# Kernel tuning notes

Hardware: AMD Instinct MI355X
Metric: run time of the kernel (lower is better)

## Reference

```python
import jax, jax.numpy as jnp
import numpy as np

# Module hyperparameters (init kwargs)
QUALITY_W = 1.0
UNCERT_W = 0.5
STEP_PEN = 0.1
EARLY_BONUS = 0.5
LATE_PEN = 0.3
ORTHO_W = 1.0

B = 8388608  # batch
MAX_STEPS = 20


def setup_inputs() -> dict:
    key = jax.random.key(0)
    ks = jax.random.split(key, 6)
    return {
        "current_quality": jax.random.uniform(ks[0], (B,), dtype=jnp.float32),
        "previous_quality": jax.random.uniform(ks[1], (B,), dtype=jnp.float32),
        "uncertainty": jax.random.uniform(ks[2], (B,), dtype=jnp.float32),
        "action": jax.random.randint(ks[3], (B,), 0, 2, dtype=jnp.int32),
        "step_count": jax.random.uniform(ks[4], (B,), dtype=jnp.float32) * MAX_STEPS,
        "final_quality": jax.random.uniform(ks[5], (B,), dtype=jnp.float32),
        "alpha": jnp.float32(1.0),
        "beta": jnp.float32(1.0),
        "gamma": jnp.float32(1.0),
        "max_steps": MAX_STEPS,
    }


def _corr(x, y):
    # torch .std() is unbiased (ddof=1)
    xm = x - x.mean()
    ym = y - y.mean()
    cov = (xm * ym).mean()
    sx = jnp.sqrt((xm * xm).sum() / (x.shape[0] - 1)) + 1e-8
    sy = jnp.sqrt((ym * ym).sum() / (y.shape[0] - 1)) + 1e-8
    return cov / (sx * sy)


def reference(current_quality, previous_quality, uncertainty, action, step_count,
              final_quality, alpha, beta, gamma, max_steps):
    ms = jnp.float32(max_steps)
    u = uncertainty

    # short-term: quality improvement
    r_short = current_quality - previous_quality

    # mid-term (vectorized form of the per-sample python loop)
    stop_r = jnp.where(u < 0.3, EARLY_BONUS, jnp.where(u > 0.7, -EARLY_BONUS, 0.0))
    cont_r = jnp.where(u > 0.5, UNCERT_W * u, -UNCERT_W * (1.0 - u))
    cont_r = cont_r - jnp.where(step_count > 0.8 * ms, LATE_PEN, 0.0)
    r_mid = jnp.where(action == 0, stop_r, cont_r) - STEP_PEN * (step_count / ms)
    # original builds r_mid via torch.tensor(list) -> detached from graph
    r_mid = jax.lax.stop_gradient(r_mid)

    # long-term
    r_long = QUALITY_W * final_quality + EARLY_BONUS * (1.0 - step_count / ms)

    total_reward = alpha * r_short + beta * r_mid + gamma * r_long

    c_sm = _corr(r_short, r_mid)
    c_sl = _corr(r_short, r_long)
    c_ml = _corr(r_mid, r_long)
    ortho_loss = ORTHO_W * (c_sm ** 2 + c_sl ** 2 + c_ml ** 2)

    return total_reward, ortho_loss, r_short, r_mid, r_long
```

## Files before the change

kernel.cpp:

```cpp
#include <hip/hip_runtime.h>
#include <math.h>

constexpr int    N       = 8388608;
constexpr int    THREADS = 256;
constexpr int    BLOCKS  = 2048;
constexpr int    VEC     = 4;
constexpr int    ITERS   = N / (BLOCKS * THREADS * VEC);
constexpr int    NSUMS   = 9;

static_assert(ITERS == 4, "grid math");

struct __attribute__((packed, aligned(4))) f4u { float x, y, z, w; };

__device__ inline void store4_u(float* p, float a, float b, float c, float d) {
    f4u v{a, b, c, d};
    *reinterpret_cast<f4u*>(p) = v;
}

__device__ inline double wave_reduce(double x) {
#pragma unroll
    for (int off = 32; off > 0; off >>= 1)
        x += __shfl_down(x, off, 64);
    return x;
}

__device__ inline void elem_compute(float cq, float pq, float u, int a, float sc, float fq,
                                    float ms, float inv_ms,
                                    float alpha, float beta, float gamma,
                                    float& rs, float& rm, float& rl, float& tot)
{
    rs = cq - pq;
    float stop_r = (u < 0.3f) ? 0.5f : ((u > 0.7f) ? -0.5f : 0.0f);
    float cont = (u > 0.5f) ? (0.5f * u) : (-0.5f * (1.0f - u));
    cont -= (sc > 0.8f * ms) ? 0.3f : 0.0f;
    float t = sc * inv_ms;
    rm = ((a == 0) ? stop_r : cont) - 0.1f * t;
    rl = fq + 0.5f * (1.0f - t);
    tot = alpha * rs + beta * rm + gamma * rl;
}

__global__ __launch_bounds__(THREADS) void reward_main(
    const float* __restrict__ cq, const float* __restrict__ pq,
    const float* __restrict__ un, const int*  __restrict__ ac,
    const float* __restrict__ sc, const float* __restrict__ fq,
    const float* __restrict__ alpha_p, const float* __restrict__ beta_p,
    const float* __restrict__ gamma_p, const int* __restrict__ ms_p,
    float* __restrict__ out, double* __restrict__ partials)
{
    const float alpha = alpha_p[0], beta = beta_p[0], gamma = gamma_p[0];
    const float ms = (float)ms_p[0];
    const float inv_ms = 1.0f / ms;

    const float4* cq4 = (const float4*)cq;
    const float4* pq4 = (const float4*)pq;
    const float4* un4 = (const float4*)un;
    const int4*   ac4 = (const int4*)ac;
    const float4* sc4 = (const float4*)sc;
    const float4* fq4 = (const float4*)fq;

    double acc[NSUMS];
#pragma unroll
    for (int s = 0; s < NSUMS; ++s) acc[s] = 0.0;

    const int tid  = blockIdx.x * THREADS + threadIdx.x;
    const int lane = threadIdx.x & 63;

#pragma unroll
    for (int it = 0; it < ITERS; ++it) {
        const int idx4 = tid + it * (BLOCKS * THREADS);
        float4 q = cq4[idx4];
        float4 p = pq4[idx4];
        float4 u = un4[idx4];
        int4   a = ac4[idx4];
        float4 s = sc4[idx4];
        float4 f = fq4[idx4];

        float qc[4] = {q.x, q.y, q.z, q.w};
        float pc[4] = {p.x, p.y, p.z, p.w};
        float uc[4] = {u.x, u.y, u.z, u.w};
        int   av[4] = {a.x, a.y, a.z, a.w};
        float sv[4] = {s.x, s.y, s.z, s.w};
        float fv[4] = {f.x, f.y, f.z, f.w};

        float rs[4], rm[4], rl[4], tt[4];
#pragma unroll
        for (int k = 0; k < 4; ++k) {
            elem_compute(qc[k], pc[k], uc[k], av[k], sv[k], fv[k],
                         ms, inv_ms, alpha, beta, gamma,
                         rs[k], rm[k], rl[k], tt[k]);
            double ds = (double)rs[k], dm = (double)rm[k], dl = (double)rl[k];
            acc[0] += ds;      acc[1] += dm;      acc[2] += dl;
            acc[3] += ds * ds; acc[4] += dm * dm; acc[5] += dl * dl;
            acc[6] += ds * dm; acc[7] += ds * dl; acc[8] += dm * dl;
        }

        const int b = idx4 * 4;

        *(float4*)(out + b) = make_float4(tt[0], tt[1], tt[2], tt[3]);

        store4_u(out +     N + 1 + b, rs[0], rs[1], rs[2], rs[3]);
        store4_u(out + 2 * N + 1 + b, rm[0], rm[1], rm[2], rm[3]);
        store4_u(out + 3 * N + 1 + b, rl[0], rl[1], rl[2], rl[3]);
    }

    __shared__ double red[NSUMS][THREADS / 64];
    const int wave = threadIdx.x >> 6;
#pragma unroll
    for (int s = 0; s < NSUMS; ++s) {
        double w = wave_reduce(acc[s]);
        if (lane == 0) red[s][wave] = w;
    }
    __syncthreads();
    if (threadIdx.x == 0) {
#pragma unroll
        for (int s = 0; s < NSUMS; ++s) {
            double t = 0.0;
#pragma unroll
            for (int w = 0; w < THREADS / 64; ++w) t += red[s][w];
            partials[blockIdx.x * NSUMS + s] = t;
        }
    }
}

__global__ __launch_bounds__(256) void reward_finish(const double* __restrict__ partials,
                                                     float* __restrict__ out)
{
    double loc[NSUMS];
#pragma unroll
    for (int s = 0; s < NSUMS; ++s) loc[s] = 0.0;
    for (int i = threadIdx.x; i < BLOCKS; i += 256) {
#pragma unroll
        for (int s = 0; s < NSUMS; ++s) loc[s] += partials[i * NSUMS + s];
    }
    __shared__ double red[NSUMS][4];
    const int lane = threadIdx.x & 63;
    const int wave = threadIdx.x >> 6;
#pragma unroll
    for (int s = 0; s < NSUMS; ++s) {
        double w = wave_reduce(loc[s]);
        if (lane == 0) red[s][wave] = w;
    }
    __syncthreads();
    if (threadIdx.x == 0) {
        double S[NSUMS];
#pragma unroll
        for (int s = 0; s < NSUMS; ++s)
            S[s] = red[s][0] + red[s][1] + red[s][2] + red[s][3];

        const double n = (double)N;
        double mx = S[0] / n, mm = S[1] / n, ml = S[2] / n;
        double cov_sm = S[6] / n - mx * mm;
        double cov_sl = S[7] / n - mx * ml;
        double cov_ml = S[8] / n - mm * ml;
        double sdS = sqrt((S[3] - n * mx * mx) / (n - 1.0)) + 1e-8;
        double sdM = sqrt((S[4] - n * mm * mm) / (n - 1.0)) + 1e-8;
        double sdL = sqrt((S[5] - n * ml * ml) / (n - 1.0)) + 1e-8;
        double c1 = cov_sm / (sdS * sdM);
        double c2 = cov_sl / (sdS * sdL);
        double c3 = cov_ml / (sdM * sdL);
        out[N] = (float)(c1 * c1 + c2 * c2 + c3 * c3);
    }
}

extern "C" void kernel_launch(void* const* d_in, const int* in_sizes, int n_in,
                              void* d_out, int out_size, void* d_ws, size_t ws_size,
                              hipStream_t stream)
{
    const float* cq   = (const float*)d_in[0];
    const float* pq   = (const float*)d_in[1];
    const float* un   = (const float*)d_in[2];
    const int*   ac   = (const int*)d_in[3];
    const float* sc   = (const float*)d_in[4];
    const float* fq   = (const float*)d_in[5];
    const float* alp  = (const float*)d_in[6];
    const float* bet  = (const float*)d_in[7];
    const float* gam  = (const float*)d_in[8];
    const int*   msp  = (const int*)d_in[9];
    float*  out      = (float*)d_out;
    double* partials = (double*)d_ws;

    reward_main<<<BLOCKS, THREADS, 0, stream>>>(cq, pq, un, ac, sc, fq,
                                                alp, bet, gam, msp, out, partials);
    reward_finish<<<1, 256, 0, stream>>>(partials, out);
}
```

Before: 309.7 us.

## Split fused reward kernel into per-output phase kernels plus stats pass

```diff
diff --git a/kernel.cpp b/kernel.cpp
--- a/kernel.cpp
+++ b/kernel.cpp
@@ -6,6 +6,7 @@
 constexpr int    BLOCKS  = 2048;
 constexpr int    VEC     = 4;
 constexpr int    ITERS   = N / (BLOCKS * THREADS * VEC);
+constexpr int    STRIDE  = BLOCKS * THREADS;
 constexpr int    NSUMS   = 9;
 
 static_assert(ITERS == 4, "grid math");
@@ -16,6 +17,9 @@
     f4u v{a, b, c, d};
     *reinterpret_cast<f4u*>(p) = v;
 }
+__device__ inline f4u load4_u(const float* p) {
+    return *reinterpret_cast<const f4u*>(p);
+}
 
 __device__ inline double wave_reduce(double x) {
 #pragma unroll
@@ -24,83 +28,114 @@
     return x;
 }
 
-__device__ inline void elem_compute(float cq, float pq, float u, int a, float sc, float fq,
-                                    float ms, float inv_ms,
-                                    float alpha, float beta, float gamma,
-                                    float& rs, float& rm, float& rl, float& tot)
-{
-    rs = cq - pq;
+
+__global__ __launch_bounds__(THREADS) void phase_rs(
+    const float* __restrict__ cq, const float* __restrict__ pq,
+    float* __restrict__ out)
+{
+    const float4* cq4 = (const float4*)cq;
+    const float4* pq4 = (const float4*)pq;
+    const int tid = blockIdx.x * THREADS + threadIdx.x;
+#pragma unroll
+    for (int it = 0; it < ITERS; ++it) {
+        const int idx4 = tid + it * STRIDE;
+        float4 q = cq4[idx4];
+        float4 p = pq4[idx4];
+        store4_u(out + N + 1 + 4 * idx4,
+                 q.x - p.x, q.y - p.y, q.z - p.z, q.w - p.w);
+    }
+}
+
+__global__ __launch_bounds__(THREADS) void phase_rl(
+    const float* __restrict__ sc, const float* __restrict__ fq,
+    const int* __restrict__ ms_p, float* __restrict__ out)
+{
+    const float ms = (float)ms_p[0];
+    const float inv_ms = 1.0f / ms;
+    const float4* sc4 = (const float4*)sc;
+    const float4* fq4 = (const float4*)fq;
+    const int tid = blockIdx.x * THREADS + threadIdx.x;
+#pragma unroll
+    for (int it = 0; it < ITERS; ++it) {
+        const int idx4 = tid + it * STRIDE;
+        float4 s = sc4[idx4];
+        float4 f = fq4[idx4];
+        store4_u(out + 3 * N + 1 + 4 * idx4,
+                 f.x + 0.5f * (1.0f - s.x * inv_ms),
+                 f.y + 0.5f * (1.0f - s.y * inv_ms),
+                 f.z + 0.5f * (1.0f - s.z * inv_ms),
+                 f.w + 0.5f * (1.0f - s.w * inv_ms));
+    }
+}
+
+__device__ inline float rm_elem(float u, int a, float sc, float ms, float inv_ms) {
     float stop_r = (u < 0.3f) ? 0.5f : ((u > 0.7f) ? -0.5f : 0.0f);
     float cont = (u > 0.5f) ? (0.5f * u) : (-0.5f * (1.0f - u));
     cont -= (sc > 0.8f * ms) ? 0.3f : 0.0f;
     float t = sc * inv_ms;
-    rm = ((a == 0) ? stop_r : cont) - 0.1f * t;
-    rl = fq + 0.5f * (1.0f - t);
-    tot = alpha * rs + beta * rm + gamma * rl;
-}
-
-__global__ __launch_bounds__(THREADS) void reward_main(
-    const float* __restrict__ cq, const float* __restrict__ pq,
-    const float* __restrict__ un, const int*  __restrict__ ac,
-    const float* __restrict__ sc, const float* __restrict__ fq,
-    const float* __restrict__ alpha_p, const float* __restrict__ beta_p,
-    const float* __restrict__ gamma_p, const int* __restrict__ ms_p,
-    float* __restrict__ out, double* __restrict__ partials)
-{
-    const float alpha = alpha_p[0], beta = beta_p[0], gamma = gamma_p[0];
+    return ((a == 0) ? stop_r : cont) - 0.1f * t;
+}
+
+__global__ __launch_bounds__(THREADS) void phase_rm(
+    const float* __restrict__ un, const int* __restrict__ ac,
+    const float* __restrict__ sc, const int* __restrict__ ms_p,
+    float* __restrict__ out)
+{
     const float ms = (float)ms_p[0];
     const float inv_ms = 1.0f / ms;
-
-    const float4* cq4 = (const float4*)cq;
-    const float4* pq4 = (const float4*)pq;
     const float4* un4 = (const float4*)un;
     const int4*   ac4 = (const int4*)ac;
     const float4* sc4 = (const float4*)sc;
-    const float4* fq4 = (const float4*)fq;
-
-    double acc[NSUMS];
-#pragma unroll
-    for (int s = 0; s < NSUMS; ++s) acc[s] = 0.0;
-
-    const int tid  = blockIdx.x * THREADS + threadIdx.x;
-    const int lane = threadIdx.x & 63;
-
-#pragma unroll
-    for (int it = 0; it < ITERS; ++it) {
-        const int idx4 = tid + it * (BLOCKS * THREADS);
-        float4 q = cq4[idx4];
-        float4 p = pq4[idx4];
+    const int tid = blockIdx.x * THREADS + threadIdx.x;
+#pragma unroll
+    for (int it = 0; it < ITERS; ++it) {
+        const int idx4 = tid + it * STRIDE;
         float4 u = un4[idx4];
         int4   a = ac4[idx4];
         float4 s = sc4[idx4];
-        float4 f = fq4[idx4];
-
-        float qc[4] = {q.x, q.y, q.z, q.w};
-        float pc[4] = {p.x, p.y, p.z, p.w};
-        float uc[4] = {u.x, u.y, u.z, u.w};
-        int   av[4] = {a.x, a.y, a.z, a.w};
-        float sv[4] = {s.x, s.y, s.z, s.w};
-        float fv[4] = {f.x, f.y, f.z, f.w};
-
-        float rs[4], rm[4], rl[4], tt[4];
+        store4_u(out + 2 * N + 1 + 4 * idx4,
+                 rm_elem(u.x, a.x, s.x, ms, inv_ms),
+                 rm_elem(u.y, a.y, s.y, ms, inv_ms),
+                 rm_elem(u.z, a.z, s.z, ms, inv_ms),
+                 rm_elem(u.w, a.w, s.w, ms, inv_ms));
+    }
+}
+
+__global__ __launch_bounds__(THREADS) void phase_tt(
+    const float* __restrict__ alpha_p, const float* __restrict__ beta_p,
+    const float* __restrict__ gamma_p,
+    float* __restrict__ out, double* __restrict__ partials)
+{
+    const float alpha = alpha_p[0], beta = beta_p[0], gamma = gamma_p[0];
+
+    double acc[NSUMS];
+#pragma unroll
+    for (int s = 0; s < NSUMS; ++s) acc[s] = 0.0;
+
+    const int tid  = blockIdx.x * THREADS + threadIdx.x;
+    const int lane = threadIdx.x & 63;
+
+#pragma unroll
+    for (int it = 0; it < ITERS; ++it) {
+        const int idx4 = tid + it * STRIDE;
+        const int b = 4 * idx4;
+        f4u rs = load4_u(out +     N + 1 + b);
+        f4u rm = load4_u(out + 2 * N + 1 + b);
+        f4u rl = load4_u(out + 3 * N + 1 + b);
+
+        float rsv[4] = {rs.x, rs.y, rs.z, rs.w};
+        float rmv[4] = {rm.x, rm.y, rm.z, rm.w};
+        float rlv[4] = {rl.x, rl.y, rl.z, rl.w};
+        float tt[4];
 #pragma unroll
         for (int k = 0; k < 4; ++k) {
-            elem_compute(qc[k], pc[k], uc[k], av[k], sv[k], fv[k],
-                         ms, inv_ms, alpha, beta, gamma,
-                         rs[k], rm[k], rl[k], tt[k]);
-            double ds = (double)rs[k], dm = (double)rm[k], dl = (double)rl[k];
+            tt[k] = alpha * rsv[k] + beta * rmv[k] + gamma * rlv[k];
+            double ds = (double)rsv[k], dm = (double)rmv[k], dl = (double)rlv[k];
             acc[0] += ds;      acc[1] += dm;      acc[2] += dl;
             acc[3] += ds * ds; acc[4] += dm * dm; acc[5] += dl * dl;
             acc[6] += ds * dm; acc[7] += ds * dl; acc[8] += dm * dl;
         }
-
-        const int b = idx4 * 4;
-
         *(float4*)(out + b) = make_float4(tt[0], tt[1], tt[2], tt[3]);
-
-        store4_u(out +     N + 1 + b, rs[0], rs[1], rs[2], rs[3]);
-        store4_u(out + 2 * N + 1 + b, rm[0], rm[1], rm[2], rm[3]);
-        store4_u(out + 3 * N + 1 + b, rl[0], rl[1], rl[2], rl[3]);
     }
 
     __shared__ double red[NSUMS][THREADS / 64];
@@ -179,7 +214,9 @@
     float*  out      = (float*)d_out;
     double* partials = (double*)d_ws;
 
-    reward_main<<<BLOCKS, THREADS, 0, stream>>>(cq, pq, un, ac, sc, fq,
-                                                alp, bet, gam, msp, out, partials);
+    phase_rs<<<BLOCKS, THREADS, 0, stream>>>(cq, pq, out);
+    phase_rl<<<BLOCKS, THREADS, 0, stream>>>(sc, fq, msp, out);
+    phase_rm<<<BLOCKS, THREADS, 0, stream>>>(un, ac, sc, msp, out);
+    phase_tt<<<BLOCKS, THREADS, 0, stream>>>(alp, bet, gam, out, partials);
     reward_finish<<<1, 256, 0, stream>>>(partials, out);
 }
```

Result: slower. 324.9 us (+4.9%).
